# Kernel tuning notes

Measured on AMD Instinct MI355X. Metric: run time of the kernel, lower is better.

The kernel has to match this reference:

```python
import math
import jax, jax.numpy as jnp
import numpy as np

B, T, C = 2, 2048, 1024
N_HEAD = 16
HEAD_DIM = C // N_HEAD


def setup_inputs() -> dict:
    key = jax.random.key(0)
    k1, k2, k3 = jax.random.split(key, 3)
    x = jax.random.normal(k1, (B, T, C), dtype=jnp.float32)
    w_attn = jax.random.normal(k2, (3 * C, C), dtype=jnp.float32) * 0.02
    w_proj = jax.random.normal(k3, (C, C), dtype=jnp.float32) * 0.02
    return {"x": x, "w_attn": w_attn, "w_proj": w_proj}


def _rope_cos_sin(seq_len, dim, dtype):
    inv_freq = 1.0 / (10000.0 ** (jnp.arange(0, dim, 2, dtype=jnp.float32) / dim))
    t = jnp.arange(seq_len, dtype=jnp.float32)
    freqs = jnp.einsum('i,j->ij', t, inv_freq)          # [T, dim/2]
    emb = jnp.concatenate([freqs, freqs], axis=-1)       # [T, dim]
    return jnp.cos(emb).astype(dtype), jnp.sin(emb).astype(dtype)


def _rotate_half(x):
    x1, x2 = jnp.split(x, 2, axis=-1)
    return jnp.concatenate([-x2, x1], axis=-1)


def _apply_rope(x, cos, sin):
    # x: [B, H, T, D]; cos/sin: [T, D] broadcast over batch/head
    return x * cos[None, None] + _rotate_half(x) * sin[None, None]


def reference(x, w_attn, w_proj):
    b, t, c = x.shape
    h, d = N_HEAD, c // N_HEAD
    qkv = x @ w_attn.T                                   # [B, T, 3C]
    q, k, v = jnp.split(qkv, 3, axis=-1)
    q = q.reshape(b, t, h, d).transpose(0, 2, 1, 3)      # [B, H, T, D]
    k = k.reshape(b, t, h, d).transpose(0, 2, 1, 3)
    v = v.reshape(b, t, h, d).transpose(0, 2, 1, 3)
    cos, sin = _rope_cos_sin(t, d, x.dtype)
    q = _apply_rope(q, cos, sin)
    k = _apply_rope(k, cos, sin)
    logits = jnp.einsum('bhqd,bhkd->bhqk', q, k) * (1.0 / math.sqrt(d))
    causal = jnp.tril(jnp.ones((t, t), dtype=bool))
    logits = jnp.where(causal[None, None], logits, jnp.float32(-jnp.inf).astype(logits.dtype))
    att = jax.nn.softmax(logits, axis=-1)                # [B, H, T, T]
    y = jnp.einsum('bhqk,bhkd->bhqd', att, v)            # [B, H, T, D]
    y = y.transpose(0, 2, 1, 3).reshape(b, t, c)
    return y @ w_proj.T
```

## Files before the change

kernel.cpp:

```cpp
#include <hip/hip_runtime.h>
#include <hip/hip_bf16.h>
#include <math.h>

#define B_ 2
#define T_ 2048
#define C_ 1024
#define H_ 16

typedef __bf16 bf16x8 __attribute__((ext_vector_type(8)));
typedef __bf16 bf16x4 __attribute__((ext_vector_type(4)));
typedef float f32x4 __attribute__((ext_vector_type(4)));
typedef float f32x16 __attribute__((ext_vector_type(16)));
typedef unsigned int u32;

#if __has_builtin(__builtin_amdgcn_exp2f)
#define EXP2(x) __builtin_amdgcn_exp2f(x)
#else
#define EXP2(x) exp2f(x)
#endif

__device__ __forceinline__ void gload16(const void* g, void* l) {
    __builtin_amdgcn_global_load_lds(
        (const __attribute__((address_space(1))) void*)g,
        (__attribute__((address_space(3))) void*)l, 16, 0, 0);
}

__device__ __forceinline__ f32x4 mfma16(bf16x8 a, bf16x8 b, f32x4 c) {
    return __builtin_amdgcn_mfma_f32_16x16x32_bf16(a, b, c, 0, 0, 0);
}
__device__ __forceinline__ f32x16 mfma32(bf16x8 a, bf16x8 b, f32x16 c) {
    return __builtin_amdgcn_mfma_f32_32x32x16_bf16(a, b, c, 0, 0, 0);
}

__device__ __forceinline__ u32 cvtpk(float lo, float hi) {
    u32 r;
    asm("v_cvt_pk_bf16_f32 %0, %1, %2" : "=v"(r) : "v"(lo), "v"(hi));
    return r;
}

__device__ __forceinline__ void plane32swap(u32& a, u32& b) {
#if __has_builtin(__builtin_amdgcn_permlane32_swap)
    auto r = __builtin_amdgcn_permlane32_swap(a, b, false, false);
    a = r[0]; b = r[1];
#else
    asm("v_permlane32_swap_b32 %0, %1" : "+v"(a), "+v"(b));
#endif
}

#define SCLQ 0.18033688011112042f
#define NLOG2_10K_32 (-0.4152410118609203f)

__global__ __launch_bounds__(256) void cast_all(const float* __restrict__ x,
                                                const float* __restrict__ wa,
                                                const float* __restrict__ wp,
                                                __bf16* __restrict__ xb,
                                                __bf16* __restrict__ wab,
                                                __bf16* __restrict__ wpb) {
    const int i = blockIdx.x * 256 + threadIdx.x;
    const float* src;
    __bf16* dst;
    int k;
    if (i < 1048576)               { src = x;  dst = xb;  k = i; }
    else if (i < 1048576 + 786432) { src = wa; dst = wab; k = i - 1048576; }
    else                           { src = wp; dst = wpb; k = i - (1048576 + 786432); }
    float4 v = ((const float4*)src)[k];
    bf16x4 o;
    o[0] = (__bf16)v.x; o[1] = (__bf16)v.y; o[2] = (__bf16)v.z; o[3] = (__bf16)v.w;
    ((bf16x4*)dst)[k] = o;
}

__global__ __launch_bounds__(256) void gemm_qkv(const __bf16* __restrict__ A,
                                                const __bf16* __restrict__ Bw,
                                                __bf16* __restrict__ Qb,
                                                __bf16* __restrict__ Kb,
                                                __bf16* __restrict__ Vt) {
    const int tid  = threadIdx.x;
    const int lane = tid & 63;
    const int w    = tid >> 6;
    const int wr = w >> 1, wc = w & 1;
    const int l15 = lane & 15, lg = lane >> 4;
    const int d0  = blockIdx.y * 24 + blockIdx.x;
    const int xcd = d0 & 7, kk0 = d0 >> 3;
    const int by  = xcd * 4 + (kk0 / 24);
    const int bx  = kk0 % 24;
    const int bm = by * 128, bn = bx * 128;
    const int K = C_;
    __shared__ __bf16 Asm[128 * 64];
    __shared__ __bf16 Bsm[128 * 64];
    f32x4 acc[4][4] = {};

    for (int kt = 0; kt < K; kt += 64) {
        if (kt) __syncthreads();
#pragma unroll
        for (int it = 0; it < 4; ++it) {
            const int c = it * 256 + tid;
            const int row = c >> 3, sg = (c & 7) ^ (row & 7);
            gload16(A  + (size_t)(bm + row) * K + kt + sg * 8, Asm + c * 8);
            gload16(Bw + (size_t)(bn + row) * K + kt + sg * 8, Bsm + c * 8);
        }
        __syncthreads();
#pragma unroll
        for (int k2 = 0; k2 < 2; ++k2) {
            bf16x8 af[4], bf[4];
#pragma unroll
            for (int i = 0; i < 4; ++i) {
                const int row = wr * 64 + i * 16 + l15;
                af[i] = *(const bf16x8*)&Asm[row * 64 + (((k2 * 4 + lg) ^ (row & 7)) * 8)];
            }
#pragma unroll
            for (int j = 0; j < 4; ++j) {
                const int row = wc * 64 + j * 16 + l15;
                bf[j] = *(const bf16x8*)&Bsm[row * 64 + (((k2 * 4 + lg) ^ (row & 7)) * 8)];
            }
#pragma unroll
            for (int i = 0; i < 4; ++i)
#pragma unroll
                for (int j = 0; j < 4; ++j)
                    acc[i][j] = mfma16(af[i], bf[j], acc[i][j]);
        }
    }
    const int region  = bn >> 10;
    const int colbase = (bn & 1023) + wc * 64;
    const int h = colbase >> 6;
    if (region < 2) {
        __bf16* dst = region ? Kb : Qb;
        const float scl = region ? 1.0f : SCLQ;
#pragma unroll
        for (int j = 0; j < 2; ++j) {
            const int d = j * 16 + l15;
            const float invf = exp2f((float)d * NLOG2_10K_32);
#pragma unroll
            for (int i = 0; i < 4; ++i)
#pragma unroll
                for (int r = 0; r < 4; ++r) {
                    const int row = bm + wr * 64 + i * 16 + lg * 4 + r;
                    const int b = row >> 11, t = row & (T_ - 1);
                    float sv, cv;
                    __sincosf((float)t * invf, &sv, &cv);
                    const float v1 = acc[i][j][r], v2 = acc[i][j + 2][r];
                    const float o1 = (v1 * cv - v2 * sv) * scl;
                    const float o2 = (v2 * cv + v1 * sv) * scl;
                    const size_t base = ((size_t)(b * H_ + h) * T_ + t) * 64;
                    dst[base + d]      = (__bf16)o1;
                    dst[base + d + 32] = (__bf16)o2;
                }
        }
    } else {
#pragma unroll
        for (int i = 0; i < 4; ++i)
#pragma unroll
            for (int j = 0; j < 4; ++j) {
                const int vcol = colbase + j * 16 + l15;
                const int hh = vcol >> 6, d = vcol & 63;
                const int row0 = bm + wr * 64 + i * 16 + lg * 4;
                const int b = row0 >> 11, t0 = row0 & (T_ - 1);
                u32 dw[2];
                dw[0] = cvtpk(acc[i][j][0], acc[i][j][1]);
                dw[1] = cvtpk(acc[i][j][2], acc[i][j][3]);
                *(uint64_t*)&Vt[((size_t)(b * H_ + hh) * 64 + d) * T_ + t0] =
                    *(uint64_t*)dw;
            }
    }
}

__global__ __launch_bounds__(256) void gemm_proj(const __bf16* __restrict__ A,
                                                 const __bf16* __restrict__ Bw,
                                                 float* __restrict__ Cp,
                                                 int N, int K) {
    const int tid  = threadIdx.x;
    const int lane = tid & 63;
    const int w    = tid >> 6;
    const int wr = w >> 1, wc = w & 1;
    const int l15 = lane & 15, lg = lane >> 4;
    const int d0  = blockIdx.y * 8 + blockIdx.x;
    const int xcd = d0 & 7, kk0 = d0 >> 3;
    const int by  = xcd * 8 + (kk0 >> 3);
    const int bx  = kk0 & 7;
    const int bm = by * 64, bn = bx * 128;
    __shared__ __bf16 Asm[64 * 64];
    __shared__ __bf16 Bsm[128 * 64];
    f32x4 acc[2][4] = {};

    for (int kt = 0; kt < K; kt += 64) {
        if (kt) __syncthreads();
#pragma unroll
        for (int it = 0; it < 2; ++it) {
            const int g = it * 256 + tid;
            const int row = g >> 3, sg = (g & 7) ^ (row & 7);
            gload16(A + (size_t)(bm + row) * K + kt + sg * 8, Asm + g * 8);
        }
#pragma unroll
        for (int it = 0; it < 4; ++it) {
            const int g = it * 256 + tid;
            const int row = g >> 3, sg = (g & 7) ^ (row & 7);
            gload16(Bw + (size_t)(bn + row) * K + kt + sg * 8, Bsm + g * 8);
        }
        __syncthreads();
#pragma unroll
        for (int k2 = 0; k2 < 2; ++k2) {
            bf16x8 af[2], bf[4];
#pragma unroll
            for (int i = 0; i < 2; ++i) {
                const int row = wr * 32 + i * 16 + l15;
                af[i] = *(const bf16x8*)&Asm[row * 64 + (((k2 * 4 + lg) ^ (row & 7)) * 8)];
            }
#pragma unroll
            for (int j = 0; j < 4; ++j) {
                const int row = wc * 64 + j * 16 + l15;
                bf[j] = *(const bf16x8*)&Bsm[row * 64 + (((k2 * 4 + lg) ^ (row & 7)) * 8)];
            }
#pragma unroll
            for (int i = 0; i < 2; ++i)
#pragma unroll
                for (int j = 0; j < 4; ++j)
                    acc[i][j] = mfma16(af[i], bf[j], acc[i][j]);
        }
    }
#pragma unroll
    for (int i = 0; i < 2; ++i)
#pragma unroll
        for (int j = 0; j < 4; ++j)
#pragma unroll
            for (int r = 0; r < 4; ++r) {
                const int row = bm + wr * 32 + i * 16 + lg * 4 + r;
                const int col = bn + wc * 64 + j * 16 + l15;
                Cp[(size_t)row * N + col] = acc[i][j][r];
            }
}

__global__ __launch_bounds__(512, 2) void attn_fwd(const __bf16* __restrict__ Qb,
                                                   const __bf16* __restrict__ Kb,
                                                   const __bf16* __restrict__ Vt,
                                                   __bf16* __restrict__ Yatt) {
    const int gid = blockIdx.x;
    const int bh = (gid & 7) * 4 + ((gid >> 3) & 3);
    const int qq = gid >> 5;
    const int qt = (qq < 8) ? (15 - qq) : (qq - 8);
    const int b = bh >> 4, h = bh & 15;
    const int tid = threadIdx.x, lane = tid & 63, w = tid >> 6;
    const int qgrp = w & 3, kvh = w >> 2;
    const int l31 = lane & 31, hi = lane >> 5;
    const int hi4 = hi * 4;
    __shared__ __bf16 Ksm[256 * 64];
    __shared__ __bf16 Vsm[64 * 256];

    const int Q0 = qt * 128 + qgrp * 32;
    const int qg = Q0 + l31;
    const __bf16* Qp = Qb + ((size_t)bh * T_ + Q0) * 64;
    const __bf16* Kp = Kb + (size_t)bh * T_ * 64;
    const __bf16* Vp = Vt + (size_t)bh * 64 * T_;

    auto STAGE = [&](int jt) {
#pragma unroll
        for (int it = 0; it < 4; ++it) {
            const int g = it * 512 + tid;
            const int kr = g >> 3, kc = (g & 7) ^ (kr & 7);
            gload16(Kp + ((size_t)(jt * 256 + kr)) * 64 + kc * 8, Ksm + g * 8);
            const int vd = g >> 5, vg = ((g & 15) ^ (vd & 15)) | (g & 16);
            gload16(Vp + (size_t)vd * T_ + jt * 256 + vg * 8, Vsm + g * 8);
        }
    };

    bf16x8 qf[4];
#pragma unroll
    for (int ds = 0; ds < 4; ++ds)
        qf[ds] = *(const bf16x8*)&Qp[l31 * 64 + ds * 16 + hi * 8];

    f32x16 otA[2] = {};
    f32x16 otB[2] = {};
    float l_run = 0.f;

    const int jmax = (qt >> 1) + 1;
    for (int jt = 0; jt < jmax; ++jt) {
        __builtin_amdgcn_s_barrier();
        STAGE(jt);
        asm volatile("s_waitcnt vmcnt(0)" ::: "memory");
        __builtin_amdgcn_s_barrier();
        __builtin_amdgcn_sched_barrier(0);

        if (jt * 256 + kvh * 128 <= Q0 + 31) {
            const bool diag = (jt == jmax - 1);
#pragma unroll
            for (int a = 0; a < 4; ++a) {
                f32x16 st = {};
#pragma unroll
                for (int ds = 0; ds < 4; ++ds) {
                    const int row = kvh * 128 + a * 32 + l31;
                    const int off = (ds * 32 + hi * 16) ^ ((row & 7) << 4);
                    bf16x8 kf = *(const bf16x8*)((const char*)Ksm + row * 128 + off);
                    st = mfma32(kf, qf[ds], st);
                }
                if (diag) {
#pragma unroll
                    for (int r = 0; r < 16; ++r) {
                        const int kv = jt * 256 + kvh * 128 + a * 32 +
                                       (r & 3) + 8 * (r >> 2) + hi4;
                        if (kv > qg) st[r] = -1e30f;
                    }
                }
                float s0 = 0.f, s1 = 0.f;
#pragma unroll
                for (int r = 0; r < 16; ++r) {
                    const float e = EXP2(st[r]);
                    st[r] = e;
                    if (r & 1) s1 += e; else s0 += e;
                }
                l_run += s0 + s1;
                u32 X0 = cvtpk(st[0], st[1]),  X1 = cvtpk(st[2], st[3]);
                u32 Y0 = cvtpk(st[4], st[5]),  Y1 = cvtpk(st[6], st[7]);
                plane32swap(X0, Y0); plane32swap(X1, Y1);
                u32 dw0[4] = {X0, X1, Y0, Y1};
                bf16x8 pa0 = *(bf16x8*)dw0;
                u32 Z0 = cvtpk(st[8], st[9]),   Z1 = cvtpk(st[10], st[11]);
                u32 W0 = cvtpk(st[12], st[13]), W1 = cvtpk(st[14], st[15]);
                plane32swap(Z0, W0); plane32swap(Z1, W1);
                u32 dw1[4] = {Z0, Z1, W0, W1};
                bf16x8 pa1 = *(bf16x8*)dw1;
#pragma unroll
                for (int db = 0; db < 2; ++db) {
                    const int row = db * 32 + l31;
                    const int g0 = (kvh * 16) | ((4 * a + hi)     ^ (row & 15));
                    const int g1 = (kvh * 16) | ((4 * a + 2 + hi) ^ (row & 15));
                    bf16x8 v0 = *(const bf16x8*)((const char*)Vsm + row * 512 + g0 * 16);
                    bf16x8 v1 = *(const bf16x8*)((const char*)Vsm + row * 512 + g1 * 16);
                    if ((a & 1) == 0) {
                        otA[db] = mfma32(v0, pa0, otA[db]);
                        otA[db] = mfma32(v1, pa1, otA[db]);
                    } else {
                        otB[db] = mfma32(v0, pa0, otB[db]);
                        otB[db] = mfma32(v1, pa1, otB[db]);
                    }
                }
            }
        }
    }
#pragma unroll
    for (int db = 0; db < 2; ++db)
#pragma unroll
        for (int r = 0; r < 16; ++r) otA[db][r] += otB[db][r];
    __builtin_amdgcn_s_barrier();
    f32x4* m4 = (f32x4*)&Ksm[0];
    float* lb = (float*)&Vsm[0];
    if (w >= 4) {
        const int woff = (w - 4) * 64 + lane;
#pragma unroll
        for (int db = 0; db < 2; ++db)
#pragma unroll
            for (int rq = 0; rq < 4; ++rq) {
                f32x4 v;
                v[0] = otA[db][rq * 4 + 0]; v[1] = otA[db][rq * 4 + 1];
                v[2] = otA[db][rq * 4 + 2]; v[3] = otA[db][rq * 4 + 3];
                m4[(db * 4 + rq) * 256 + woff] = v;
            }
        lb[woff] = l_run;
    }
    __builtin_amdgcn_s_barrier();
    if (w < 4) {
        const int woff = w * 64 + lane;
#pragma unroll
        for (int db = 0; db < 2; ++db)
#pragma unroll
            for (int rq = 0; rq < 4; ++rq) {
                f32x4 v = m4[(db * 4 + rq) * 256 + woff];
                otA[db][rq * 4 + 0] += v[0]; otA[db][rq * 4 + 1] += v[1];
                otA[db][rq * 4 + 2] += v[2]; otA[db][rq * 4 + 3] += v[3];
            }
        l_run += lb[woff];
        l_run += __shfl_xor(l_run, 32);
        const float inv = 1.f / l_run;
        __bf16* Yp = Yatt + ((size_t)(b * T_ + qg)) * C_ + h * 64;
#pragma unroll
        for (int db = 0; db < 2; ++db)
#pragma unroll
            for (int rq = 0; rq < 4; ++rq) {
                const int r = rq * 4;
                u32 dw[2];
                dw[0] = cvtpk(otA[db][r] * inv,     otA[db][r + 1] * inv);
                dw[1] = cvtpk(otA[db][r + 2] * inv, otA[db][r + 3] * inv);
                const int d = db * 32 + 8 * rq + hi4;
                *(uint64_t*)&Yp[d] = *(uint64_t*)dw;
            }
    }
}

extern "C" void kernel_launch(void* const* d_in, const int* in_sizes, int n_in,
                              void* d_out, int out_size, void* d_ws, size_t ws_size,
                              hipStream_t stream) {
    const float* x      = (const float*)d_in[0];
    const float* w_attn = (const float*)d_in[1];
    const float* w_proj = (const float*)d_in[2];
    float* out = (float*)d_out;
    char* ws = (char*)d_ws;

    __bf16* xb  = (__bf16*)(ws);
    __bf16* wab = (__bf16*)(ws + 8388608);
    __bf16* wpb = (__bf16*)(ws + 14680064);
    __bf16* Qb  = (__bf16*)(ws + 16777216);
    __bf16* Kb  = (__bf16*)(ws + 25165824);
    __bf16* Vt  = (__bf16*)(ws + 33554432);
    __bf16* Ya  = (__bf16*)(ws + 41943040);

    cast_all<<<dim3(8192), 256, 0, stream>>>(x, w_attn, w_proj, xb, wab, wpb);

    gemm_qkv<<<dim3(3 * C_ / 128, B_ * T_ / 128), 256, 0, stream>>>(
        xb, wab, Qb, Kb, Vt);

    attn_fwd<<<dim3(16 * 32), 512, 0, stream>>>(Qb, Kb, Vt, Ya);

    gemm_proj<<<dim3(C_ / 128, B_ * T_ / 64), 256, 0, stream>>>(
        Ya, wpb, out, C_, C_);
}
```

Before: 97.07 us.

## Read K and V directly from global memory in attention, dropping LDS staging

The attention kernel no longer stages 256-row K and V tiles into shared memory with barriers on every iteration. Each wave now loads its K rows and V-transposed rows straight from global memory, one 32-key chunk at a time, and the two KV-half wave groups interleave chunks of four. Shared memory is kept only for the final cross-wave reduction. This removes the per-tile block barriers and the LDS round trip, and skips keys above the causal bound per wave rather than per tile. The cost is redundant global and L2 traffic, since the four query groups each read the same K and V, and global load latency is now exposed inside the MFMA loop.

```diff
diff --git a/kernel.cpp b/kernel.cpp
--- a/kernel.cpp
+++ b/kernel.cpp
@@ -241,8 +241,8 @@
     const int qgrp = w & 3, kvh = w >> 2;
     const int l31 = lane & 31, hi = lane >> 5;
     const int hi4 = hi * 4;
-    __shared__ __bf16 Ksm[256 * 64];
-    __shared__ __bf16 Vsm[64 * 256];
+    __shared__ f32x4 m4[8 * 256];
+    __shared__ float lb[256];
 
     const int Q0 = qt * 128 + qgrp * 32;
     const int qg = Q0 + l31;
@@ -250,17 +250,6 @@
     const __bf16* Kp = Kb + (size_t)bh * T_ * 64;
     const __bf16* Vp = Vt + (size_t)bh * 64 * T_;
 
-    auto STAGE = [&](int jt) {
-#pragma unroll
-        for (int it = 0; it < 4; ++it) {
-            const int g = it * 512 + tid;
-            const int kr = g >> 3, kc = (g & 7) ^ (kr & 7);
-            gload16(Kp + ((size_t)(jt * 256 + kr)) * 64 + kc * 8, Ksm + g * 8);
-            const int vd = g >> 5, vg = ((g & 15) ^ (vd & 15)) | (g & 16);
-            gload16(Vp + (size_t)vd * T_ + jt * 256 + vg * 8, Vsm + g * 8);
-        }
-    };
-
     bf16x8 qf[4];
 #pragma unroll
     for (int ds = 0; ds < 4; ++ds)
@@ -270,67 +259,57 @@
     f32x16 otB[2] = {};
     float l_run = 0.f;
 
-    const int jmax = (qt >> 1) + 1;
-    for (int jt = 0; jt < jmax; ++jt) {
-        __builtin_amdgcn_s_barrier();
-        STAGE(jt);
-        asm volatile("s_waitcnt vmcnt(0)" ::: "memory");
-        __builtin_amdgcn_s_barrier();
-        __builtin_amdgcn_sched_barrier(0);
-
-        if (jt * 256 + kvh * 128 <= Q0 + 31) {
-            const bool diag = (jt == jmax - 1);
-#pragma unroll
-            for (int a = 0; a < 4; ++a) {
-                f32x16 st = {};
-#pragma unroll
-                for (int ds = 0; ds < 4; ++ds) {
-                    const int row = kvh * 128 + a * 32 + l31;
-                    const int off = (ds * 32 + hi * 16) ^ ((row & 7) << 4);
-                    bf16x8 kf = *(const bf16x8*)((const char*)Ksm + row * 128 + off);
-                    st = mfma32(kf, qf[ds], st);
+    const int cmax = qt * 4 + qgrp;
+    for (int cb = kvh * 4; cb <= cmax; cb += 8) {
+#pragma unroll
+        for (int cc = 0; cc < 4; ++cc) {
+            const int c = cb + cc;
+            if (c > cmax) break;
+            const int kv0 = c * 32;
+            f32x16 st = {};
+            const __bf16* Krow = Kp + (size_t)(kv0 + l31) * 64 + hi * 8;
+#pragma unroll
+            for (int ds = 0; ds < 4; ++ds) {
+                bf16x8 kf = *(const bf16x8*)(Krow + ds * 16);
+                st = mfma32(kf, qf[ds], st);
+            }
+            if (c == cmax) {
+#pragma unroll
+                for (int r = 0; r < 16; ++r) {
+                    const int kv = kv0 + (r & 3) + 8 * (r >> 2) + hi4;
+                    if (kv > qg) st[r] = -1e30f;
                 }
-                if (diag) {
-#pragma unroll
-                    for (int r = 0; r < 16; ++r) {
-                        const int kv = jt * 256 + kvh * 128 + a * 32 +
-                                       (r & 3) + 8 * (r >> 2) + hi4;
-                        if (kv > qg) st[r] = -1e30f;
-                    }
+            }
+            float s0 = 0.f, s1 = 0.f;
+#pragma unroll
+            for (int r = 0; r < 16; ++r) {
+                const float e = EXP2(st[r]);
+                st[r] = e;
+                if (r & 1) s1 += e; else s0 += e;
+            }
+            l_run += s0 + s1;
+            u32 X0 = cvtpk(st[0], st[1]),  X1 = cvtpk(st[2], st[3]);
+            u32 Y0 = cvtpk(st[4], st[5]),  Y1 = cvtpk(st[6], st[7]);
+            plane32swap(X0, Y0); plane32swap(X1, Y1);
+            u32 dw0[4] = {X0, X1, Y0, Y1};
+            bf16x8 pa0 = *(bf16x8*)dw0;
+            u32 Z0 = cvtpk(st[8], st[9]),   Z1 = cvtpk(st[10], st[11]);
+            u32 W0 = cvtpk(st[12], st[13]), W1 = cvtpk(st[14], st[15]);
+            plane32swap(Z0, W0); plane32swap(Z1, W1);
+            u32 dw1[4] = {Z0, Z1, W0, W1};
+            bf16x8 pa1 = *(bf16x8*)dw1;
+#pragma unroll
+            for (int db = 0; db < 2; ++db) {
+                const __bf16* Vrow = Vp + (size_t)(db * 32 + l31) * T_ + kv0 + hi * 8;
+                bf16x8 v0 = *(const bf16x8*)(Vrow);
+                bf16x8 v1 = *(const bf16x8*)(Vrow + 16);
+                if ((c & 1) == 0) {
+                    otA[db] = mfma32(v0, pa0, otA[db]);
+                    otA[db] = mfma32(v1, pa1, otA[db]);
+                } else {
+                    otB[db] = mfma32(v0, pa0, otB[db]);
+                    otB[db] = mfma32(v1, pa1, otB[db]);
                 }
-                float s0 = 0.f, s1 = 0.f;
-#pragma unroll
-                for (int r = 0; r < 16; ++r) {
-                    const float e = EXP2(st[r]);
-                    st[r] = e;
-                    if (r & 1) s1 += e; else s0 += e;
-                }
-                l_run += s0 + s1;
-                u32 X0 = cvtpk(st[0], st[1]),  X1 = cvtpk(st[2], st[3]);
-                u32 Y0 = cvtpk(st[4], st[5]),  Y1 = cvtpk(st[6], st[7]);
-                plane32swap(X0, Y0); plane32swap(X1, Y1);
-                u32 dw0[4] = {X0, X1, Y0, Y1};
-                bf16x8 pa0 = *(bf16x8*)dw0;
-                u32 Z0 = cvtpk(st[8], st[9]),   Z1 = cvtpk(st[10], st[11]);
-                u32 W0 = cvtpk(st[12], st[13]), W1 = cvtpk(st[14], st[15]);
-                plane32swap(Z0, W0); plane32swap(Z1, W1);
-                u32 dw1[4] = {Z0, Z1, W0, W1};
-                bf16x8 pa1 = *(bf16x8*)dw1;
-#pragma unroll
-                for (int db = 0; db < 2; ++db) {
-                    const int row = db * 32 + l31;
-                    const int g0 = (kvh * 16) | ((4 * a + hi)     ^ (row & 15));
-                    const int g1 = (kvh * 16) | ((4 * a + 2 + hi) ^ (row & 15));
-                    bf16x8 v0 = *(const bf16x8*)((const char*)Vsm + row * 512 + g0 * 16);
-                    bf16x8 v1 = *(const bf16x8*)((const char*)Vsm + row * 512 + g1 * 16);
-                    if ((a & 1) == 0) {
-                        otA[db] = mfma32(v0, pa0, otA[db]);
-                        otA[db] = mfma32(v1, pa1, otA[db]);
-                    } else {
-                        otB[db] = mfma32(v0, pa0, otB[db]);
-                        otB[db] = mfma32(v1, pa1, otB[db]);
-                    }
-                }
             }
         }
     }
@@ -338,9 +317,7 @@
     for (int db = 0; db < 2; ++db)
 #pragma unroll
         for (int r = 0; r < 16; ++r) otA[db][r] += otB[db][r];
-    __builtin_amdgcn_s_barrier();
-    f32x4* m4 = (f32x4*)&Ksm[0];
-    float* lb = (float*)&Vsm[0];
+    __syncthreads();
     if (w >= 4) {
         const int woff = (w - 4) * 64 + lane;
 #pragma unroll
@@ -354,7 +331,7 @@
             }
         lb[woff] = l_run;
     }
-    __builtin_amdgcn_s_barrier();
+    __syncthreads();
     if (w < 4) {
         const int woff = w * 64 + lane;
 #pragma unroll
```

New measurement: 125.0 us. 1.29x slower.
